# Optimization experiments

Hardware: AMD Instinct MI355X
Metric: run time of the kernel (lower is better)

The kernel has to match this reference:

```python
import jax, jax.numpy as jnp
import numpy as np

L_THETAS = (1.0, 0.2, 0.1)
LR = 1.0
C = 10      # num_out_caps
D = 16      # vector_depth
M = 10      # transformation matrices per capsule


def setup_inputs() -> dict:
    key = jax.random.key(0)
    k_in, k_w, k_dc = jax.random.split(key, 3)
    B, H, Wd, F, DIN = 64, 14, 14, 32, 8
    N = H * Wd * F
    inputs = jax.random.normal(k_in, (B, H, Wd, F, DIN), dtype=jnp.float32)
    # glorot-uniform for W: shape [N, input_d, d*m]
    fan_in, fan_out = DIN, D * M
    limit = float(np.sqrt(6.0 / (fan_in + fan_out)))
    W = jax.random.uniform(k_w, (N, DIN, D * M), minval=-limit, maxval=limit, dtype=jnp.float32)
    # digit_caps codebook: RandomUniform(-1, 1), shape [c, d]
    digit_caps = jax.random.uniform(k_dc, (C, D), minval=-1.0, maxval=1.0, dtype=jnp.float32)
    return {"inputs": inputs, "W": W, "digit_caps": digit_caps}


def reference(inputs, W, digit_caps):
    B = inputs.shape[0]
    H, Wd, F, DIN = inputs.shape[1:]
    N = H * Wd * F
    c, d = digit_caps.shape
    m = W.shape[-1] // d

    x = inputs.reshape(B, N, DIN)
    # per-capsule transformation: [B, N, d*m] -> [B, N*m, d]
    u = jnp.einsum('bji,jik->bjk', x, W).reshape(B, N * m, d)
    # squash-like nonlinearity: tanh(|u|)/|u| * u
    n = jnp.linalg.norm(u, axis=-1, keepdims=True)
    u = (jnp.tanh(n) / n) * u

    # Similarities u . digit_caps[c]; the original tiles u over c, but since the
    # winner-take-all mask is constant along d, sum((u*mask_c)*dc) == mask_c * (u.dc).
    sim0 = jnp.einsum('bnd,cd->bnc', u, digit_caps)  # [B, Nm, c]
    mask = jnp.ones_like(sim0)
    accum = jnp.zeros_like(digit_caps)               # sum of sparse updates, reduced over (b, n)
    for theta in L_THETAS:
        sims = sim0 * mask
        winners = jnp.argmax(sims, axis=-1)                        # [B, Nm]
        onehot = jax.nn.one_hot(winners, c, dtype=u.dtype)         # [B, Nm, c]
        # sum_{b,n} onehot * (u - dc) == einsum(onehot, u) - count_c * dc
        accum = accum + (LR * theta) * (
            jnp.einsum('bnc,bnd->cd', onehot, u)
            - jnp.sum(onehot, axis=(0, 1))[:, None] * digit_caps
        )
        mask = mask - onehot

    updates = accum / (B * N * m)   # mean over axes [0, 1] of the [B,Nm,c,d] update tensor
    dc = digit_caps + updates
    dc = dc / jnp.linalg.norm(dc, axis=-1, keepdims=True)

    sim_final = jnp.einsum('bnd,cd->bnc', u, dc)     # [B, Nm, c]
    return jax.nn.softmax(jnp.mean(sim_final, axis=-2), axis=-1)  # [B, c]
```

## Files before the change

kernel.cpp:

```cpp
#include <hip/hip_runtime.h>
#include <hip/hip_fp16.h>
#include <math.h>

#define NPOS 6272
#define DIN_ 8
#define DVEC 16
#define CCAP 10
#define JC 4
#define NBLK (NPOS / JC)
#define PSTRIDE 1200
#define ACC_FLOATS 1194
#define P_OFF 1280
#define SH_WORDS 5760

__device__ __forceinline__ float fdot2u(unsigned a, unsigned b, float c) {
#if __has_builtin(__builtin_amdgcn_fdot2)
    typedef _Float16 h2v __attribute__((ext_vector_type(2)));
    return __builtin_amdgcn_fdot2(__builtin_bit_cast(h2v, a),
                                  __builtin_bit_cast(h2v, b), c, false);
#else
    __half2 p = __hmul2(__builtin_bit_cast(__half2, a), __builtin_bit_cast(__half2, b));
    return c + (__low2float(p) + __high2float(p));
#endif
}
__device__ __forceinline__ unsigned pack_rn(float lo, float hi) {
    return __builtin_bit_cast(unsigned, __floats2half2_rn(lo, hi));
}
__device__ __forceinline__ unsigned umaxu(unsigned a, unsigned b) { return a > b ? a : b; }

__device__ __forceinline__ unsigned qsum_h2(unsigned v) {
    int t = __builtin_amdgcn_mov_dpp((int)v, 0xB1, 0xF, 0xF, true);
    __half2 a = __builtin_bit_cast(__half2, v);
    __half2 b = __builtin_bit_cast(__half2, (unsigned)t);
    a = __hadd2(a, b);
    v = __builtin_bit_cast(unsigned, a);
    t = __builtin_amdgcn_mov_dpp((int)v, 0x4E, 0xF, 0xF, true);
    b = __builtin_bit_cast(__half2, (unsigned)t);
    a = __builtin_bit_cast(__half2, v);
    a = __hadd2(a, b);
    return __builtin_bit_cast(unsigned, a);
}
__device__ __forceinline__ float qsum_f32(float v) {
    int t = __builtin_amdgcn_mov_dpp(__builtin_bit_cast(int, v), 0xB1, 0xF, 0xF, true);
    v += __builtin_bit_cast(float, t);
    t = __builtin_amdgcn_mov_dpp(__builtin_bit_cast(int, v), 0x4E, 0xF, 0xF, true);
    v += __builtin_bit_cast(float, t);
    return v;
}

__device__ __forceinline__ float squash_scale(float nsq) {
    float n = __builtin_amdgcn_sqrtf(nsq);
    float e = __expf(2.0f * n);
    float th = 1.0f - 2.0f * __builtin_amdgcn_rcpf(e + 1.0f);
    return th * __builtin_amdgcn_rcpf(n);
}

__global__ __launch_bounds__(256) void caps_main(
    const float* __restrict__ xin,
    const float* __restrict__ Wg,
    const float* __restrict__ dcg,
    float* __restrict__ P,
    float* __restrict__ ACC)
{
    __shared__ __align__(16) unsigned SH[SH_WORDS];
    __shared__ __align__(16) unsigned dch[84];
    __shared__ __align__(16) unsigned ub_out[4][64][8];

    const int tid  = threadIdx.x;
    const int lane = tid & 63;
    const int wvu  = __builtin_amdgcn_readfirstlane(tid >> 6);
    const int j0   = blockIdx.x * JC;
    const int j    = j0 + wvu;

    for (int g = tid; g < 640; g += 256) {
        int jk = g / 40, d4 = g - jk * 40;
        int jj = jk >> 2, k = jk & 3;
        const float* s1 = Wg + (size_t)(j0 + jj) * 1280 + (2 * k) * 160 + d4 * 4;
        float4 a = *(const float4*)s1;
        float4 b = *(const float4*)(s1 + 160);
        uint4 w;
        w.x = pack_rn(a.x, b.x); w.y = pack_rn(a.y, b.y);
        w.z = pack_rn(a.z, b.z); w.w = pack_rn(a.w, b.w);
        *(uint4*)(SH + jk * 160 + d4 * 4) = w;
    }
    if (tid < 20) {
        int c = tid >> 1, part = tid & 1;
        const float4* dp = (const float4*)(dcg + c * 16 + part * 8);
        float4 a = dp[0], b = dp[1];
        uint4 w;
        w.x = pack_rn(a.x, a.y); w.y = pack_rn(a.z, a.w);
        w.z = pack_rn(b.x, b.y); w.w = pack_rn(b.z, b.w);
        *(uint4*)(dch + c * 8 + part * 4) = w;
    }

    unsigned xh[4];
    {
        const float4* xp = (const float4*)(xin + (size_t)lane * (NPOS * DIN_)
                                               + (size_t)j * DIN_);
        float4 xa = xp[0], xb = xp[1];
        xh[0] = pack_rn(xa.x, xa.y); xh[1] = pack_rn(xa.z, xa.w);
        xh[2] = pack_rn(xb.x, xb.y); xh[3] = pack_rn(xb.z, xb.w);
    }
    __syncthreads();

    __half2 S[CCAP][8];
    float   T[CCAP];
    __half2 ub[8];
    #pragma unroll
    for (int c = 0; c < CCAP; ++c) {
        T[c] = 0.0f;
        #pragma unroll
        for (int k = 0; k < 8; ++k) S[c][k] = __float2half2_rn(0.0f);
    }
    #pragma unroll
    for (int k = 0; k < 8; ++k) ub[k] = __float2half2_rn(0.0f);

    const unsigned* wbase = SH + wvu * 640;
    const unsigned MASKHI = 0xFFFFFFF0u;

    #pragma unroll 1
    for (int m = 0; m < 10; ++m) {
        float u[DVEC];
        #pragma unroll
        for (int d = 0; d < DVEC; ++d) u[d] = 0.0f;
        #pragma unroll
        for (int k = 0; k < 4; ++k) {
            const uint4* wk = (const uint4*)(wbase + k * 160 + m * 16);
            uint4 q0 = wk[0], q1 = wk[1], q2 = wk[2], q3 = wk[3];
            unsigned xk = xh[k];
            u[0]  = fdot2u(xk, q0.x, u[0]);  u[1]  = fdot2u(xk, q0.y, u[1]);
            u[2]  = fdot2u(xk, q0.z, u[2]);  u[3]  = fdot2u(xk, q0.w, u[3]);
            u[4]  = fdot2u(xk, q1.x, u[4]);  u[5]  = fdot2u(xk, q1.y, u[5]);
            u[6]  = fdot2u(xk, q1.z, u[6]);  u[7]  = fdot2u(xk, q1.w, u[7]);
            u[8]  = fdot2u(xk, q2.x, u[8]);  u[9]  = fdot2u(xk, q2.y, u[9]);
            u[10] = fdot2u(xk, q2.z, u[10]); u[11] = fdot2u(xk, q2.w, u[11]);
            u[12] = fdot2u(xk, q3.x, u[12]); u[13] = fdot2u(xk, q3.y, u[13]);
            u[14] = fdot2u(xk, q3.z, u[14]); u[15] = fdot2u(xk, q3.w, u[15]);
        }

        unsigned uh[8];
        #pragma unroll
        for (int k = 0; k < 8; ++k) uh[k] = pack_rn(u[2 * k], u[2 * k + 1]);

        float sb[CCAP];
        #pragma unroll
        for (int c = 0; c < CCAP; ++c) {
            const uint4* dq = (const uint4*)(dch + c * 8);
            uint4 e0 = dq[0], e1 = dq[1];
            float acc = fdot2u(uh[0], e0.x, 64.0f);
            acc = fdot2u(uh[1], e0.y, acc);
            acc = fdot2u(uh[2], e0.z, acc);
            acc = fdot2u(uh[3], e0.w, acc);
            acc = fdot2u(uh[4], e1.x, acc);
            acc = fdot2u(uh[5], e1.y, acc);
            acc = fdot2u(uh[6], e1.z, acc);
            acc = fdot2u(uh[7], e1.w, acc);
            sb[c] = acc;
        }

        float nsq = fdot2u(uh[0], uh[0], 0.0f);
        nsq = fdot2u(uh[1], uh[1], nsq);
        nsq = fdot2u(uh[2], uh[2], nsq);
        nsq = fdot2u(uh[3], uh[3], nsq);
        float nsqb = fdot2u(uh[4], uh[4], 0.0f);
        nsqb = fdot2u(uh[5], uh[5], nsqb);
        nsqb = fdot2u(uh[6], uh[6], nsqb);
        nsqb = fdot2u(uh[7], uh[7], nsqb);
        float sc = squash_scale(nsq + nsqb);

        unsigned pe[CCAP], p1[CCAP], p2[CCAP];
        #pragma unroll
        for (int c = 0; c < CCAP; ++c)
            pe[c] = (__builtin_bit_cast(unsigned, sb[c]) & MASKHI) | (unsigned)(15 - c);

        unsigned m0 = pe[0];
        #pragma unroll
        for (int c = 1; c < CCAP; ++c) m0 = umaxu(m0, pe[c]);

        #pragma unroll
        for (int c = 0; c < CCAP; ++c) {
            const unsigned zc = 0x42800000u | (unsigned)(15 - c);
            p1[c] = (pe[c] == m0) ? zc : pe[c];
        }
        unsigned m1 = p1[0];
        #pragma unroll
        for (int c = 1; c < CCAP; ++c) m1 = umaxu(m1, p1[c]);

        #pragma unroll
        for (int c = 0; c < CCAP; ++c) {
            const unsigned zc = 0x42800000u | (unsigned)(15 - c);
            unsigned ne = (__builtin_bit_cast(unsigned, 128.0f - sb[c]) & MASKHI)
                          | (unsigned)(15 - c);
            unsigned fresh = (m1 == zc) ? ne : zc;
            p2[c] = (p1[c] == m1) ? fresh : p1[c];
        }
        unsigned m2 = p2[0];
        #pragma unroll
        for (int c = 1; c < CCAP; ++c) m2 = umaxu(m2, p2[c]);

        __half2 sch = __float2half2_rn(sc);
        #pragma unroll
        for (int k = 0; k < 8; ++k)
            ub[k] = __hfma2(sch, __builtin_bit_cast(__half2, uh[k]), ub[k]);

        #pragma unroll
        for (int c = 0; c < CCAP; ++c) {
            float w = (pe[c] == m0 ? 1.0f : 0.0f);
            w += (p1[c] == m1) ? 0.2f : 0.0f;
            w += (p2[c] == m2) ? 0.1f : 0.0f;
            T[c] += w;
            __half2 wh = __float2half2_rn(w * sc);
            #pragma unroll
            for (int k = 0; k < 8; ++k)
                S[c][k] = __hfma2(wh, __builtin_bit_cast(__half2, uh[k]), S[c][k]);
        }
    }

    __syncthreads();

    {
        unsigned sq[CCAP][8];
        float tq[CCAP];
        #pragma unroll
        for (int c = 0; c < CCAP; ++c) {
            tq[c] = qsum_f32(T[c]);
            #pragma unroll
            for (int k = 0; k < 8; ++k)
                sq[c][k] = qsum_h2(__builtin_bit_cast(unsigned, S[c][k]));
        }
        if ((lane & 3) == 0) {
            unsigned* row = SH + (wvu * 16 + (lane >> 2)) * 90;
            #pragma unroll
            for (int c = 0; c < CCAP; ++c) {
                #pragma unroll
                for (int k = 0; k < 8; ++k) row[c * 8 + k] = sq[c][k];
                row[80 + c] = __builtin_bit_cast(unsigned, tq[c]);
            }
        }
        #pragma unroll
        for (int k = 0; k < 8; ++k)
            ub_out[wvu][lane][k] = __builtin_bit_cast(unsigned, ub[k]);
    }
    __syncthreads();

    if (P != nullptr) {
        float* prow = P + (size_t)blockIdx.x * PSTRIDE;
        for (int q = tid; q < ACC_FLOATS; q += 256) {
            float v = 0.0f;
            if (q < 160) {
                int wd = (q >> 4) * 8 + ((q & 15) >> 1);
                int hi = q & 1;
                #pragma unroll 8
                for (int r = 0; r < 64; ++r) {
                    __half2 h = __builtin_bit_cast(__half2, SH[r * 90 + wd]);
                    v += hi ? __high2float(h) : __low2float(h);
                }
            } else if (q < 170) {
                #pragma unroll 8
                for (int r = 0; r < 64; ++r)
                    v += __builtin_bit_cast(float, SH[r * 90 + 80 + (q - 160)]);
            } else {
                int x = q - 170, b = x >> 4, d = x & 15;
                #pragma unroll
                for (int w2 = 0; w2 < 4; ++w2) {
                    __half2 h = __builtin_bit_cast(__half2, ub_out[w2][b][d >> 1]);
                    v += (d & 1) ? __high2float(h) : __low2float(h);
                }
            }
            prow[q] = v;
        }
    } else {
        for (int q = tid; q < ACC_FLOATS; q += 256) {
            float v = 0.0f;
            if (q < 160) {
                int wd = (q >> 4) * 8 + ((q & 15) >> 1);
                int hi = q & 1;
                #pragma unroll 8
                for (int r = 0; r < 64; ++r) {
                    __half2 h = __builtin_bit_cast(__half2, SH[r * 90 + wd]);
                    v += hi ? __high2float(h) : __low2float(h);
                }
            } else if (q < 170) {
                #pragma unroll 8
                for (int r = 0; r < 64; ++r)
                    v += __builtin_bit_cast(float, SH[r * 90 + 80 + (q - 160)]);
            } else {
                int x = q - 170, b = x >> 4, d = x & 15;
                #pragma unroll
                for (int w2 = 0; w2 < 4; ++w2) {
                    __half2 h = __builtin_bit_cast(__half2, ub_out[w2][b][d >> 1]);
                    v += (d & 1) ? __high2float(h) : __low2float(h);
                }
            }
            unsafeAtomicAdd(&ACC[q], v);
        }
    }
}

__global__ __launch_bounds__(256) void caps_reduce(const float* __restrict__ P,
                                                   float* __restrict__ ACC)
{
    const int t = threadIdx.x;
    float acc[5] = {0.f, 0.f, 0.f, 0.f, 0.f};
    const int r0 = blockIdx.x * 16;
    for (int r = 0; r < 16; ++r) {
        const float* row = P + (size_t)(r0 + r) * PSTRIDE;
        #pragma unroll
        for (int s = 0; s < 5; ++s) {
            int col = t + 256 * s;
            float v = (col < ACC_FLOATS) ? row[col] : 0.0f;
            acc[s] += v;
        }
    }
    #pragma unroll
    for (int s = 0; s < 5; ++s) {
        int col = t + 256 * s;
        if (col < ACC_FLOATS) unsafeAtomicAdd(&ACC[col], acc[s]);
    }
}

__global__ __launch_bounds__(256) void caps_final(const float* __restrict__ ACC,
                                                  const float* __restrict__ dcg,
                                                  float* __restrict__ outp)
{
    __shared__ float dcn[160];
    __shared__ float rnm[10];
    __shared__ float lg[640];
    const int t = threadIdx.x;

    if (t < 160) {
        int c = t >> 4;
        float d0 = dcg[t];
        float upd = (ACC[t] - ACC[160 + c] * d0) * (float)(1.0 / 4014080.0);
        dcn[t] = d0 + upd;
    }
    __syncthreads();
    if (t < 10) {
        float s = 0.0f;
        #pragma unroll
        for (int d = 0; d < 16; ++d) s += dcn[t * 16 + d] * dcn[t * 16 + d];
        rnm[t] = 1.0f / sqrtf(s);
    }
    __syncthreads();
    if (t < 160) dcn[t] *= rnm[t >> 4];
    __syncthreads();

    for (int q = t; q < 640; q += 256) {
        int b = q / 10, c = q - 10 * b;
        const float* ubp = &ACC[170 + b * 16];
        float s = 0.0f;
        #pragma unroll
        for (int d = 0; d < 16; ++d) s += ubp[d] * dcn[c * 16 + d];
        lg[q] = s * (float)(1.0 / 62720.0);
    }
    __syncthreads();
    if (t < 64) {
        float mx = lg[t * 10];
        #pragma unroll
        for (int c = 1; c < 10; ++c) mx = fmaxf(mx, lg[t * 10 + c]);
        float e[10];
        float ssum = 0.0f;
        #pragma unroll
        for (int c = 0; c < 10; ++c) { e[c] = expf(lg[t * 10 + c] - mx); ssum += e[c]; }
        float inv = 1.0f / ssum;
        #pragma unroll
        for (int c = 0; c < 10; ++c) outp[t * 10 + c] = e[c] * inv;
    }
}

extern "C" void kernel_launch(void* const* d_in, const int* in_sizes, int n_in,
                              void* d_out, int out_size, void* d_ws, size_t ws_size,
                              hipStream_t stream)
{
    const float* xin = (const float*)d_in[0];
    const float* Wg  = (const float*)d_in[1];
    const float* dcg = (const float*)d_in[2];
    float* outp = (float*)d_out;
    float* ws = (float*)d_ws;
    float* ACC = ws;

    const size_t need = (size_t)(P_OFF + (size_t)NBLK * PSTRIDE) * sizeof(float);
    float* P = (ws_size >= need) ? (ws + P_OFF) : nullptr;

    hipMemsetAsync(ACC, 0, ACC_FLOATS * sizeof(float), stream);
    caps_main<<<dim3(NBLK), dim3(256), 0, stream>>>(xin, Wg, dcg, P, ACC);
    if (P) caps_reduce<<<dim3(98), dim3(256), 0, stream>>>(P, ACC);
    caps_final<<<dim3(1), dim3(256), 0, stream>>>(ACC, dcg, outp);
}
```

Before: 105.0 us.

## Precompute W·digit_caps per position to get similarities directly from x

The code folds digit_caps into W by precomputing, per position and matrix m, the projection W_m·dc_c for each input-dim pair. Similarities then take 4 dot2 ops on x per capsule instead of 8 on the packed u, and they no longer wait on u being computed. The precompute does extra global reads of W and fp32 FMAs per block, and it changes rounding because sims now come from pre-squash u via fp16 projections. The winner-selection code is also reorganised to reuse one array and build the weights incrementally, which lowers register pressure.

```diff
diff --git a/kernel.cpp b/kernel.cpp
--- a/kernel.cpp
+++ b/kernel.cpp
@@ -12,6 +12,7 @@
 #define ACC_FLOATS 1194
 #define P_OFF 1280
 #define SH_WORDS 5760
+#define VOFF 2560
 
 __device__ __forceinline__ float fdot2u(unsigned a, unsigned b, float c) {
 #if __has_builtin(__builtin_amdgcn_fdot2)
@@ -63,7 +64,6 @@
     float* __restrict__ ACC)
 {
     __shared__ __align__(16) unsigned SH[SH_WORDS];
-    __shared__ __align__(16) unsigned dch[84];
     __shared__ __align__(16) unsigned ub_out[4][64][8];
 
     const int tid  = threadIdx.x;
@@ -83,14 +83,27 @@
         w.z = pack_rn(a.z, b.z); w.w = pack_rn(a.w, b.w);
         *(uint4*)(SH + jk * 160 + d4 * 4) = w;
     }
-    if (tid < 20) {
-        int c = tid >> 1, part = tid & 1;
-        const float4* dp = (const float4*)(dcg + c * 16 + part * 8);
-        float4 a = dp[0], b = dp[1];
-        uint4 w;
-        w.x = pack_rn(a.x, a.y); w.y = pack_rn(a.z, a.w);
-        w.z = pack_rn(b.x, b.y); w.w = pack_rn(b.z, b.w);
-        *(uint4*)(dch + c * 8 + part * 4) = w;
+
+    {
+        const float* wrow = Wg + (size_t)j * 1280;
+        for (int e = lane; e < 400; e += 64) {
+            int mm = e / 40;
+            int rest = e - mm * 40;
+            int c = rest >> 2, k = rest & 3;
+            const float4* w0 = (const float4*)(wrow + (2 * k) * 160 + mm * 16);
+            const float4* w1 = (const float4*)(wrow + (2 * k + 1) * 160 + mm * 16);
+            const float4* dp = (const float4*)(dcg + c * 16);
+            float v0 = 0.0f, v1 = 0.0f;
+            #pragma unroll
+            for (int d4 = 0; d4 < 4; ++d4) {
+                float4 a = w0[d4], b = w1[d4], dd = dp[d4];
+                v0 = fmaf(a.x, dd.x, v0); v0 = fmaf(a.y, dd.y, v0);
+                v0 = fmaf(a.z, dd.z, v0); v0 = fmaf(a.w, dd.w, v0);
+                v1 = fmaf(b.x, dd.x, v1); v1 = fmaf(b.y, dd.y, v1);
+                v1 = fmaf(b.z, dd.z, v1); v1 = fmaf(b.w, dd.w, v1);
+            }
+            SH[VOFF + wvu * 400 + e] = pack_rn(v0, v1);
+        }
     }
 
     unsigned xh[4];
@@ -116,10 +129,25 @@
     for (int k = 0; k < 8; ++k) ub[k] = __float2half2_rn(0.0f);
 
     const unsigned* wbase = SH + wvu * 640;
+    const unsigned* vbase0 = SH + VOFF + wvu * 400;
     const unsigned MASKHI = 0xFFFFFFF0u;
 
     #pragma unroll 1
     for (int m = 0; m < 10; ++m) {
+        float sb[CCAP];
+        {
+            const unsigned* vb = vbase0 + m * 40;
+            #pragma unroll
+            for (int c = 0; c < CCAP; ++c) {
+                uint4 vv = *(const uint4*)(vb + c * 4);
+                float acc = fdot2u(xh[0], vv.x, 64.0f);
+                acc = fdot2u(xh[1], vv.y, acc);
+                acc = fdot2u(xh[2], vv.z, acc);
+                acc = fdot2u(xh[3], vv.w, acc);
+                sb[c] = acc;
+            }
+        }
+
         float u[DVEC];
         #pragma unroll
         for (int d = 0; d < DVEC; ++d) u[d] = 0.0f;
@@ -142,22 +170,6 @@
         #pragma unroll
         for (int k = 0; k < 8; ++k) uh[k] = pack_rn(u[2 * k], u[2 * k + 1]);
 
-        float sb[CCAP];
-        #pragma unroll
-        for (int c = 0; c < CCAP; ++c) {
-            const uint4* dq = (const uint4*)(dch + c * 8);
-            uint4 e0 = dq[0], e1 = dq[1];
-            float acc = fdot2u(uh[0], e0.x, 64.0f);
-            acc = fdot2u(uh[1], e0.y, acc);
-            acc = fdot2u(uh[2], e0.z, acc);
-            acc = fdot2u(uh[3], e0.w, acc);
-            acc = fdot2u(uh[4], e1.x, acc);
-            acc = fdot2u(uh[5], e1.y, acc);
-            acc = fdot2u(uh[6], e1.z, acc);
-            acc = fdot2u(uh[7], e1.w, acc);
-            sb[c] = acc;
-        }
-
         float nsq = fdot2u(uh[0], uh[0], 0.0f);
         nsq = fdot2u(uh[1], uh[1], nsq);
         nsq = fdot2u(uh[2], uh[2], nsq);
@@ -168,7 +180,8 @@
         nsqb = fdot2u(uh[7], uh[7], nsqb);
         float sc = squash_scale(nsq + nsqb);
 
-        unsigned pe[CCAP], p1[CCAP], p2[CCAP];
+        unsigned pe[CCAP];
+        float w[CCAP];
         #pragma unroll
         for (int c = 0; c < CCAP; ++c)
             pe[c] = (__builtin_bit_cast(unsigned, sb[c]) & MASKHI) | (unsigned)(15 - c);
@@ -176,27 +189,31 @@
         unsigned m0 = pe[0];
         #pragma unroll
         for (int c = 1; c < CCAP; ++c) m0 = umaxu(m0, pe[c]);
-
         #pragma unroll
         for (int c = 0; c < CCAP; ++c) {
             const unsigned zc = 0x42800000u | (unsigned)(15 - c);
-            p1[c] = (pe[c] == m0) ? zc : pe[c];
-        }
-        unsigned m1 = p1[0];
-        #pragma unroll
-        for (int c = 1; c < CCAP; ++c) m1 = umaxu(m1, p1[c]);
-
+            bool e0 = (pe[c] == m0);
+            w[c] = e0 ? 1.0f : 0.0f;
+            pe[c] = e0 ? zc : pe[c];
+        }
+        unsigned m1 = pe[0];
+        #pragma unroll
+        for (int c = 1; c < CCAP; ++c) m1 = umaxu(m1, pe[c]);
         #pragma unroll
         for (int c = 0; c < CCAP; ++c) {
             const unsigned zc = 0x42800000u | (unsigned)(15 - c);
             unsigned ne = (__builtin_bit_cast(unsigned, 128.0f - sb[c]) & MASKHI)
                           | (unsigned)(15 - c);
+            bool e1 = (pe[c] == m1);
+            w[c] += e1 ? 0.2f : 0.0f;
             unsigned fresh = (m1 == zc) ? ne : zc;
-            p2[c] = (p1[c] == m1) ? fresh : p1[c];
-        }
-        unsigned m2 = p2[0];
-        #pragma unroll
-        for (int c = 1; c < CCAP; ++c) m2 = umaxu(m2, p2[c]);
+            pe[c] = e1 ? fresh : pe[c];
+        }
+        unsigned m2 = pe[0];
+        #pragma unroll
+        for (int c = 1; c < CCAP; ++c) m2 = umaxu(m2, pe[c]);
+        #pragma unroll
+        for (int c = 0; c < CCAP; ++c) w[c] += (pe[c] == m2) ? 0.1f : 0.0f;
 
         __half2 sch = __float2half2_rn(sc);
         #pragma unroll
@@ -205,11 +222,8 @@
 
         #pragma unroll
         for (int c = 0; c < CCAP; ++c) {
-            float w = (pe[c] == m0 ? 1.0f : 0.0f);
-            w += (p1[c] == m1) ? 0.2f : 0.0f;
-            w += (p2[c] == m2) ? 0.1f : 0.0f;
-            T[c] += w;
-            __half2 wh = __float2half2_rn(w * sc);
+            T[c] += w[c];
+            __half2 wh = __float2half2_rn(w[c] * sc);
             #pragma unroll
             for (int k = 0; k < 8; ++k)
                 S[c][k] = __hfma2(wh, __builtin_bit_cast(__half2, uh[k]), S[c][k]);
```

Result: slower. 127.9 us (+21.8%).

## Process two capsule positions per wave to halve block count and partials

Applied to the files above, without the earlier changes.

Each block now handles 8 capsule positions instead of 4. Every wave loops over two positions and keeps its S/T accumulators in registers across both, so there are half as many blocks and half as many per-block partials for the reduce kernel, which is relaunched with 49 blocks instead of 98. The winner-take-all bookkeeping is also rewritten to reuse one pe array and build the weights incrementally, which cuts register pressure. In exchange, per-block work becomes serial and fewer blocks are available to fill the GPU (784 instead of 1568), and shared-memory use for W doubles to fill SH.

```diff
diff --git a/kernel.cpp b/kernel.cpp
--- a/kernel.cpp
+++ b/kernel.cpp
@@ -6,7 +6,7 @@
 #define DIN_ 8
 #define DVEC 16
 #define CCAP 10
-#define JC 4
+#define JC 8
 #define NBLK (NPOS / JC)
 #define PSTRIDE 1200
 #define ACC_FLOATS 1194
@@ -70,9 +70,8 @@
     const int lane = tid & 63;
     const int wvu  = __builtin_amdgcn_readfirstlane(tid >> 6);
     const int j0   = blockIdx.x * JC;
-    const int j    = j0 + wvu;
-
-    for (int g = tid; g < 640; g += 256) {
+
+    for (int g = tid; g < 1280; g += 256) {
         int jk = g / 40, d4 = g - jk * 40;
         int jj = jk >> 2, k = jk & 3;
         const float* s1 = Wg + (size_t)(j0 + jj) * 1280 + (2 * k) * 160 + d4 * 4;
@@ -93,13 +92,14 @@
         *(uint4*)(dch + c * 8 + part * 4) = w;
     }
 
-    unsigned xh[4];
-    {
+    unsigned xh2[2][4];
+    #pragma unroll
+    for (int jj2 = 0; jj2 < 2; ++jj2) {
         const float4* xp = (const float4*)(xin + (size_t)lane * (NPOS * DIN_)
-                                               + (size_t)j * DIN_);
+                                               + (size_t)(j0 + wvu + 4 * jj2) * DIN_);
         float4 xa = xp[0], xb = xp[1];
-        xh[0] = pack_rn(xa.x, xa.y); xh[1] = pack_rn(xa.z, xa.w);
-        xh[2] = pack_rn(xb.x, xb.y); xh[3] = pack_rn(xb.z, xb.w);
+        xh2[jj2][0] = pack_rn(xa.x, xa.y); xh2[jj2][1] = pack_rn(xa.z, xa.w);
+        xh2[jj2][2] = pack_rn(xb.x, xb.y); xh2[jj2][3] = pack_rn(xb.z, xb.w);
     }
     __syncthreads();
 
@@ -115,104 +115,113 @@
     #pragma unroll
     for (int k = 0; k < 8; ++k) ub[k] = __float2half2_rn(0.0f);
 
-    const unsigned* wbase = SH + wvu * 640;
     const unsigned MASKHI = 0xFFFFFFF0u;
 
     #pragma unroll 1
-    for (int m = 0; m < 10; ++m) {
-        float u[DVEC];
-        #pragma unroll
-        for (int d = 0; d < DVEC; ++d) u[d] = 0.0f;
-        #pragma unroll
-        for (int k = 0; k < 4; ++k) {
-            const uint4* wk = (const uint4*)(wbase + k * 160 + m * 16);
-            uint4 q0 = wk[0], q1 = wk[1], q2 = wk[2], q3 = wk[3];
-            unsigned xk = xh[k];
-            u[0]  = fdot2u(xk, q0.x, u[0]);  u[1]  = fdot2u(xk, q0.y, u[1]);
-            u[2]  = fdot2u(xk, q0.z, u[2]);  u[3]  = fdot2u(xk, q0.w, u[3]);
-            u[4]  = fdot2u(xk, q1.x, u[4]);  u[5]  = fdot2u(xk, q1.y, u[5]);
-            u[6]  = fdot2u(xk, q1.z, u[6]);  u[7]  = fdot2u(xk, q1.w, u[7]);
-            u[8]  = fdot2u(xk, q2.x, u[8]);  u[9]  = fdot2u(xk, q2.y, u[9]);
-            u[10] = fdot2u(xk, q2.z, u[10]); u[11] = fdot2u(xk, q2.w, u[11]);
-            u[12] = fdot2u(xk, q3.x, u[12]); u[13] = fdot2u(xk, q3.y, u[13]);
-            u[14] = fdot2u(xk, q3.z, u[14]); u[15] = fdot2u(xk, q3.w, u[15]);
-        }
-
-        unsigned uh[8];
-        #pragma unroll
-        for (int k = 0; k < 8; ++k) uh[k] = pack_rn(u[2 * k], u[2 * k + 1]);
-
-        float sb[CCAP];
-        #pragma unroll
-        for (int c = 0; c < CCAP; ++c) {
-            const uint4* dq = (const uint4*)(dch + c * 8);
-            uint4 e0 = dq[0], e1 = dq[1];
-            float acc = fdot2u(uh[0], e0.x, 64.0f);
-            acc = fdot2u(uh[1], e0.y, acc);
-            acc = fdot2u(uh[2], e0.z, acc);
-            acc = fdot2u(uh[3], e0.w, acc);
-            acc = fdot2u(uh[4], e1.x, acc);
-            acc = fdot2u(uh[5], e1.y, acc);
-            acc = fdot2u(uh[6], e1.z, acc);
-            acc = fdot2u(uh[7], e1.w, acc);
-            sb[c] = acc;
-        }
-
-        float nsq = fdot2u(uh[0], uh[0], 0.0f);
-        nsq = fdot2u(uh[1], uh[1], nsq);
-        nsq = fdot2u(uh[2], uh[2], nsq);
-        nsq = fdot2u(uh[3], uh[3], nsq);
-        float nsqb = fdot2u(uh[4], uh[4], 0.0f);
-        nsqb = fdot2u(uh[5], uh[5], nsqb);
-        nsqb = fdot2u(uh[6], uh[6], nsqb);
-        nsqb = fdot2u(uh[7], uh[7], nsqb);
-        float sc = squash_scale(nsq + nsqb);
-
-        unsigned pe[CCAP], p1[CCAP], p2[CCAP];
-        #pragma unroll
-        for (int c = 0; c < CCAP; ++c)
-            pe[c] = (__builtin_bit_cast(unsigned, sb[c]) & MASKHI) | (unsigned)(15 - c);
-
-        unsigned m0 = pe[0];
-        #pragma unroll
-        for (int c = 1; c < CCAP; ++c) m0 = umaxu(m0, pe[c]);
-
-        #pragma unroll
-        for (int c = 0; c < CCAP; ++c) {
-            const unsigned zc = 0x42800000u | (unsigned)(15 - c);
-            p1[c] = (pe[c] == m0) ? zc : pe[c];
-        }
-        unsigned m1 = p1[0];
-        #pragma unroll
-        for (int c = 1; c < CCAP; ++c) m1 = umaxu(m1, p1[c]);
-
-        #pragma unroll
-        for (int c = 0; c < CCAP; ++c) {
-            const unsigned zc = 0x42800000u | (unsigned)(15 - c);
-            unsigned ne = (__builtin_bit_cast(unsigned, 128.0f - sb[c]) & MASKHI)
-                          | (unsigned)(15 - c);
-            unsigned fresh = (m1 == zc) ? ne : zc;
-            p2[c] = (p1[c] == m1) ? fresh : p1[c];
-        }
-        unsigned m2 = p2[0];
-        #pragma unroll
-        for (int c = 1; c < CCAP; ++c) m2 = umaxu(m2, p2[c]);
-
-        __half2 sch = __float2half2_rn(sc);
-        #pragma unroll
-        for (int k = 0; k < 8; ++k)
-            ub[k] = __hfma2(sch, __builtin_bit_cast(__half2, uh[k]), ub[k]);
-
-        #pragma unroll
-        for (int c = 0; c < CCAP; ++c) {
-            float w = (pe[c] == m0 ? 1.0f : 0.0f);
-            w += (p1[c] == m1) ? 0.2f : 0.0f;
-            w += (p2[c] == m2) ? 0.1f : 0.0f;
-            T[c] += w;
-            __half2 wh = __float2half2_rn(w * sc);
+    for (int jj2 = 0; jj2 < 2; ++jj2) {
+        const unsigned* wbase = SH + (wvu + 4 * jj2) * 640;
+        unsigned xh[4];
+        #pragma unroll
+        for (int k = 0; k < 4; ++k) xh[k] = xh2[jj2][k];
+
+        #pragma unroll 1
+        for (int m = 0; m < 10; ++m) {
+            float u[DVEC];
+            #pragma unroll
+            for (int d = 0; d < DVEC; ++d) u[d] = 0.0f;
+            #pragma unroll
+            for (int k = 0; k < 4; ++k) {
+                const uint4* wk = (const uint4*)(wbase + k * 160 + m * 16);
+                uint4 q0 = wk[0], q1 = wk[1], q2 = wk[2], q3 = wk[3];
+                unsigned xk = xh[k];
+                u[0]  = fdot2u(xk, q0.x, u[0]);  u[1]  = fdot2u(xk, q0.y, u[1]);
+                u[2]  = fdot2u(xk, q0.z, u[2]);  u[3]  = fdot2u(xk, q0.w, u[3]);
+                u[4]  = fdot2u(xk, q1.x, u[4]);  u[5]  = fdot2u(xk, q1.y, u[5]);
+                u[6]  = fdot2u(xk, q1.z, u[6]);  u[7]  = fdot2u(xk, q1.w, u[7]);
+                u[8]  = fdot2u(xk, q2.x, u[8]);  u[9]  = fdot2u(xk, q2.y, u[9]);
+                u[10] = fdot2u(xk, q2.z, u[10]); u[11] = fdot2u(xk, q2.w, u[11]);
+                u[12] = fdot2u(xk, q3.x, u[12]); u[13] = fdot2u(xk, q3.y, u[13]);
+                u[14] = fdot2u(xk, q3.z, u[14]); u[15] = fdot2u(xk, q3.w, u[15]);
+            }
+
+            unsigned uh[8];
+            #pragma unroll
+            for (int k = 0; k < 8; ++k) uh[k] = pack_rn(u[2 * k], u[2 * k + 1]);
+
+            float sb[CCAP];
+            #pragma unroll
+            for (int c = 0; c < CCAP; ++c) {
+                const uint4* dq = (const uint4*)(dch + c * 8);
+                uint4 e0 = dq[0], e1 = dq[1];
+                float acc = fdot2u(uh[0], e0.x, 64.0f);
+                acc = fdot2u(uh[1], e0.y, acc);
+                acc = fdot2u(uh[2], e0.z, acc);
+                acc = fdot2u(uh[3], e0.w, acc);
+                acc = fdot2u(uh[4], e1.x, acc);
+                acc = fdot2u(uh[5], e1.y, acc);
+                acc = fdot2u(uh[6], e1.z, acc);
+                acc = fdot2u(uh[7], e1.w, acc);
+                sb[c] = acc;
+            }
+
+            float nsq = fdot2u(uh[0], uh[0], 0.0f);
+            nsq = fdot2u(uh[1], uh[1], nsq);
+            nsq = fdot2u(uh[2], uh[2], nsq);
+            nsq = fdot2u(uh[3], uh[3], nsq);
+            float nsqb = fdot2u(uh[4], uh[4], 0.0f);
+            nsqb = fdot2u(uh[5], uh[5], nsqb);
+            nsqb = fdot2u(uh[6], uh[6], nsqb);
+            nsqb = fdot2u(uh[7], uh[7], nsqb);
+            float sc = squash_scale(nsq + nsqb);
+
+            unsigned pe[CCAP];
+            float w[CCAP];
+            #pragma unroll
+            for (int c = 0; c < CCAP; ++c)
+                pe[c] = (__builtin_bit_cast(unsigned, sb[c]) & MASKHI) | (unsigned)(15 - c);
+
+            unsigned m0 = pe[0];
+            #pragma unroll
+            for (int c = 1; c < CCAP; ++c) m0 = umaxu(m0, pe[c]);
+            #pragma unroll
+            for (int c = 0; c < CCAP; ++c) {
+                const unsigned zc = 0x42800000u | (unsigned)(15 - c);
+                bool e0 = (pe[c] == m0);
+                w[c] = e0 ? 1.0f : 0.0f;
+                pe[c] = e0 ? zc : pe[c];
+            }
+            unsigned m1 = pe[0];
+            #pragma unroll
+            for (int c = 1; c < CCAP; ++c) m1 = umaxu(m1, pe[c]);
+            #pragma unroll
+            for (int c = 0; c < CCAP; ++c) {
+                const unsigned zc = 0x42800000u | (unsigned)(15 - c);
+                unsigned ne = (__builtin_bit_cast(unsigned, 128.0f - sb[c]) & MASKHI)
+                              | (unsigned)(15 - c);
+                bool e1 = (pe[c] == m1);
+                w[c] += e1 ? 0.2f : 0.0f;
+                unsigned fresh = (m1 == zc) ? ne : zc;
+                pe[c] = e1 ? fresh : pe[c];
+            }
+            unsigned m2 = pe[0];
+            #pragma unroll
+            for (int c = 1; c < CCAP; ++c) m2 = umaxu(m2, pe[c]);
+            #pragma unroll
+            for (int c = 0; c < CCAP; ++c) w[c] += (pe[c] == m2) ? 0.1f : 0.0f;
+
+            __half2 sch = __float2half2_rn(sc);
             #pragma unroll
             for (int k = 0; k < 8; ++k)
-                S[c][k] = __hfma2(wh, __builtin_bit_cast(__half2, uh[k]), S[c][k]);
+                ub[k] = __hfma2(sch, __builtin_bit_cast(__half2, uh[k]), ub[k]);
+
+            #pragma unroll
+            for (int c = 0; c < CCAP; ++c) {
+                T[c] += w[c];
+                __half2 wh = __float2half2_rn(w[c] * sc);
+                #pragma unroll
+                for (int k = 0; k < 8; ++k)
+                    S[c][k] = __hfma2(wh, __builtin_bit_cast(__half2, uh[k]), S[c][k]);
+            }
         }
     }
 
@@ -384,6 +393,6 @@
 
     hipMemsetAsync(ACC, 0, ACC_FLOATS * sizeof(float), stream);
     caps_main<<<dim3(NBLK), dim3(256), 0, stream>>>(xin, Wg, dcg, P, ACC);
-    if (P) caps_reduce<<<dim3(98), dim3(256), 0, stream>>>(P, ACC);
+    if (P) caps_reduce<<<dim3(49), dim3(256), 0, stream>>>(P, ACC);
     caps_final<<<dim3(1), dim3(256), 0, stream>>>(ACC, dcg, outp);
 }
```

Result: slower. 110.9 us (+5.6%).
